# Optimization experiments

Hardware: AMD Instinct MI355X
Metric: run time of the kernel (lower is better)

The kernel has to match this reference:

```python
import jax, jax.numpy as jnp
import numpy as np

ALPHA = 0.1
BETA = 0.1
N_TASKS = 8
N_ROBOTS = 3
B = 2097152


def setup_inputs() -> dict:
    key = jax.random.key(0)
    k1, k2, k3, k4 = jax.random.split(key, 4)
    predictions = jax.random.normal(k1, (B, N_TASKS * N_ROBOTS), dtype=jnp.float32)
    targets = jax.random.uniform(k2, (B, N_TASKS * N_ROBOTS), dtype=jnp.float32)
    R = jax.random.uniform(k3, (B, N_TASKS, N_ROBOTS), dtype=jnp.float32)  # task capability requirements
    Q = jax.random.uniform(k4, (B, N_ROBOTS, N_ROBOTS), dtype=jnp.float32)  # per-robot capability rows
    return {"predictions": predictions, "targets": targets, "R": R, "Q": Q}


def reference(predictions, targets, R, Q):
    # BCEWithLogitsLoss (mean): softplus(x) - x * t
    base_loss = jnp.mean(jax.nn.softplus(predictions) - predictions * targets)

    b = predictions.shape[0]
    pred_m = predictions.reshape(b, N_TASKS, N_ROBOTS)  # [B, 8, 3]
    # robot assigned to task iff prediction > 0.5 (hard threshold, as in original)
    assigned = (pred_m > 0.5).astype(predictions.dtype)  # [B, 8, 3]
    # total capability per task: sum of Q rows of assigned robots
    total_capability = jnp.einsum('btr,brc->btc', assigned, Q)  # [B, 8, 3]
    shortage = jnp.maximum(R - total_capability, 0.0).sum(-1)  # [B, 8]
    # original only counts tasks where the raw prediction row-sum is > 0
    active = pred_m.sum(-1) > 0.0  # [B, 8]
    capability_violation = jnp.where(active, shortage, 0.0).sum() / b

    time_violation = jnp.asarray(0.0, dtype=predictions.dtype)
    total_loss = base_loss + ALPHA * capability_violation + BETA * time_violation
    return (total_loss, base_loss, capability_violation, time_violation)
```

## Files before the change

### kernel.cpp

```cpp
#include <hip/hip_runtime.h>

#define N_TASKS 8
#define ROW 24
#define ROWB 96
#define TILE 64
#define QROWB 36

typedef __attribute__((address_space(3))) void* lds_ptr_t;
typedef const __attribute__((address_space(1))) void* gbl_ptr_t;

#define PRED0 0
#define R0    512
#define Q0    1024
#define BUFSZ 1168

#define SB0 __builtin_amdgcn_sched_barrier(0)
#define WAITV25 do { asm volatile("s_waitcnt vmcnt(25)" ::: "memory"); } while (0)
#define WAITV0  do { asm volatile("s_waitcnt vmcnt(0)"  ::: "memory"); } while (0)

#define STAGE(TILEIDX, BSEL) do {                                              \
    const char* _predT = (const char*)pred + (size_t)(TILEIDX) * (TILE * ROWB);\
    const char* _RT    = (const char*)Rm   + (size_t)(TILEIDX) * (TILE * ROWB);\
    const char* _QT    = (const char*)Qm   + (size_t)(TILEIDX) * (TILE * QROWB);\
    _Pragma("unroll")                                                          \
    for (int _j = 0; _j < 8; ++_j)                                             \
        __builtin_amdgcn_global_load_lds((gbl_ptr_t)(_predT + _j * 768 + srcPR),\
                                         (lds_ptr_t)(&bufL[BSEL][PRED0 + _j * 64]), 16, 0, 0);\
    _Pragma("unroll")                                                          \
    for (int _j = 0; _j < 8; ++_j)                                             \
        __builtin_amdgcn_global_load_lds((gbl_ptr_t)(_RT + _j * 768 + srcPR),  \
                                         (lds_ptr_t)(&bufL[BSEL][R0 + _j * 64]), 16, 0, 0);\
    __builtin_amdgcn_global_load_lds((gbl_ptr_t)(_QT + l * 16),                \
                                     (lds_ptr_t)(&bufL[BSEL][Q0]), 16, 0, 0);  \
    __builtin_amdgcn_global_load_lds((gbl_ptr_t)(_QT + 1024 + l * 16),         \
                                     (lds_ptr_t)(&bufL[BSEL][Q0 + 64]), 16, 0, 0);\
    __builtin_amdgcn_global_load_lds((gbl_ptr_t)(_QT + 2048 + l * 4),          \
                                     (lds_ptr_t)(&bufL[BSEL][Q0 + 128]), 4, 0, 0);\
} while (0)

#define LOADT(TT, TILEIDX) do {                                                \
    const char* _targT = (const char*)targ + (size_t)(TILEIDX) * (TILE * ROWB);\
    _Pragma("unroll")                                                          \
    for (int _j = 0; _j < 6; ++_j)                                             \
        TT[_j] = *(const float4*)(_targT + (_j * 64 + l) * 16);                \
} while (0)

#define COMPUTE(BSEL, TT) do {                                                 \
    const float4* _predL = &bufL[BSEL][PRED0];                                 \
    const float4* _RL    = &bufL[BSEL][R0];                                    \
    const float* _qbase  = (const float*)&bufL[BSEL][Q0];                      \
    float pv[ROW];                                                             \
    _Pragma("unroll")                                                          \
    for (int _s = 0; _s < 6; ++_s) {                                           \
        float4 _v = _predL[8 * l + (_s ^ key)];                                \
        pv[4 * _s + 0] = _v.x; pv[4 * _s + 1] = _v.y;                          \
        pv[4 * _s + 2] = _v.z; pv[4 * _s + 3] = _v.w;                          \
    }                                                                          \
    float _sp0 = 0.0f, _sp1 = 0.0f;                                            \
    _Pragma("unroll")                                                          \
    for (int _i = 0; _i < ROW; _i += 2) {                                      \
        _sp0 += fmaxf(pv[_i],     0.0f) + __logf(1.0f + __expf(-fabsf(pv[_i])));\
        _sp1 += fmaxf(pv[_i + 1], 0.0f) + __logf(1.0f + __expf(-fabsf(pv[_i + 1])));\
    }                                                                          \
    float rv[ROW];                                                             \
    _Pragma("unroll")                                                          \
    for (int _s = 0; _s < 6; ++_s) {                                           \
        float4 _v = _RL[8 * l + (_s ^ key)];                                   \
        rv[4 * _s + 0] = _v.x; rv[4 * _s + 1] = _v.y;                          \
        rv[4 * _s + 2] = _v.z; rv[4 * _s + 3] = _v.w;                          \
    }                                                                          \
    float qv[9];                                                               \
    _Pragma("unroll")                                                          \
    for (int _e = 0; _e < 9; ++_e) qv[_e] = _qbase[9 * l + _e];                \
    float _cap = 0.0f;                                                         \
    _Pragma("unroll")                                                          \
    for (int _tk = 0; _tk < N_TASKS; ++_tk) {                                  \
        float _p0 = pv[_tk * 3 + 0];                                           \
        float _p1 = pv[_tk * 3 + 1];                                           \
        float _p2 = pv[_tk * 3 + 2];                                           \
        float _a0 = (_p0 > 0.5f) ? 1.0f : 0.0f;                                \
        float _a1 = (_p1 > 0.5f) ? 1.0f : 0.0f;                                \
        float _a2 = (_p2 > 0.5f) ? 1.0f : 0.0f;                                \
        float _tc0 = _a0 * qv[0] + _a1 * qv[3] + _a2 * qv[6];                  \
        float _tc1 = _a0 * qv[1] + _a1 * qv[4] + _a2 * qv[7];                  \
        float _tc2 = _a0 * qv[2] + _a1 * qv[5] + _a2 * qv[8];                  \
        float _sh  = fmaxf(rv[_tk * 3 + 0] - _tc0, 0.0f)                       \
                   + fmaxf(rv[_tk * 3 + 1] - _tc1, 0.0f)                       \
                   + fmaxf(rv[_tk * 3 + 2] - _tc2, 0.0f);                      \
        bool _active = (_p0 + _p1 + _p2) > 0.0f;                               \
        _cap += _active ? _sh : 0.0f;                                          \
    }                                                                          \
    float _dt0 = 0.0f, _dt1 = 0.0f;                                            \
    _Pragma("unroll")                                                          \
    for (int _j = 0; _j < 6; ++_j) {                                           \
        float4 _pw = _predL[pieceIdx[_j]];                                     \
        _dt0 += _pw.x * TT[_j].x + _pw.y * TT[_j].y;                           \
        _dt1 += _pw.z * TT[_j].z + _pw.w * TT[_j].w;                           \
    }                                                                          \
    base_acc += (double)((_sp0 + _sp1) - (_dt0 + _dt1));                       \
    cap_acc  += (double)_cap;                                                  \
} while (0)

__global__ __launch_bounds__(64) void mrta_partial_kernel(
    const float* __restrict__ pred,
    const float* __restrict__ targ,
    const float* __restrict__ Rm,
    const float* __restrict__ Qm,
    double* __restrict__ partials,
    int B)
{
    __shared__ __align__(16) float4 bufL[2][BUFSZ];

    const int l = threadIdx.x;

    int sfix = (l & 7) ^ (l >> 3);
    if (sfix >= 6) sfix = l & 1;
    const int srcPR = ROWB * (l >> 3) + 16 * sfix;

    int pieceIdx[6];
#pragma unroll
    for (int j = 0; j < 6; ++j) {
        int g = j * 64 + l;
        int r = g / 6;
        int s = g - r * 6;
        pieceIdx[j] = 8 * r + (s ^ (r & 7));
    }
    const int key = l & 7;

    double base_acc = 0.0, cap_acc = 0.0;

    const int G = gridDim.x;
    const int ntiles = B / TILE;
    const int t0 = blockIdx.x;
    const int n = (t0 < ntiles) ? ((ntiles - t0 + G - 1) / G) : 0;

    float4 ttA[6], ttB[6];

    if (n > 0) { STAGE(t0, 0); LOADT(ttA, t0); }

    for (int i = 0; i < n; i += 2) {
        const int tcur = t0 + i * G;
        {
            if (i + 1 < n) {
                const int tnext = tcur + G;
                STAGE(tnext, 1); LOADT(ttB, tnext);
                SB0; WAITV25; SB0;
            } else {
                SB0; WAITV0; SB0;
            }
            COMPUTE(0, ttA);
            SB0;
        }
        if (i + 1 < n) {
            if (i + 2 < n) {
                const int tnn = tcur + 2 * G;
                STAGE(tnn, 0); LOADT(ttA, tnn);
                SB0; WAITV25; SB0;
            } else {
                SB0; WAITV0; SB0;
            }
            COMPUTE(1, ttB);
            SB0;
        }
    }

    if (blockIdx.x == 0) {
        int row = ntiles * TILE + l;
        if (row < B) {
            const float* pr = pred + (size_t)row * ROW;
            const float* tr = targ + (size_t)row * ROW;
            const float* rr = Rm   + (size_t)row * ROW;
            const float* qr = Qm   + (size_t)row * 9;
            float base = 0.0f;
            float pv[ROW];
            for (int i = 0; i < ROW; ++i) {
                float x = pr[i];
                pv[i] = x;
                base += fmaxf(x, 0.0f) + __logf(1.0f + __expf(-fabsf(x))) - x * tr[i];
            }
            float cap = 0.0f;
            for (int tk = 0; tk < N_TASKS; ++tk) {
                float p0 = pv[tk * 3 + 0], p1 = pv[tk * 3 + 1], p2 = pv[tk * 3 + 2];
                float a0 = (p0 > 0.5f) ? 1.0f : 0.0f;
                float a1 = (p1 > 0.5f) ? 1.0f : 0.0f;
                float a2 = (p2 > 0.5f) ? 1.0f : 0.0f;
                float tc0 = a0 * qr[0] + a1 * qr[3] + a2 * qr[6];
                float tc1 = a0 * qr[1] + a1 * qr[4] + a2 * qr[7];
                float tc2 = a0 * qr[2] + a1 * qr[5] + a2 * qr[8];
                float sh  = fmaxf(rr[tk * 3 + 0] - tc0, 0.0f)
                          + fmaxf(rr[tk * 3 + 1] - tc1, 0.0f)
                          + fmaxf(rr[tk * 3 + 2] - tc2, 0.0f);
                if ((p0 + p1 + p2) > 0.0f) cap += sh;
            }
            base_acc += (double)base;
            cap_acc  += (double)cap;
        }
    }

#pragma unroll
    for (int off = 32; off > 0; off >>= 1) {
        base_acc += __shfl_down(base_acc, off);
        cap_acc  += __shfl_down(cap_acc, off);
    }
    if (l == 0) {
        partials[blockIdx.x]             = base_acc;
        partials[gridDim.x + blockIdx.x] = cap_acc;
    }
}

__global__ __launch_bounds__(256) void mrta_final_kernel(
    const double* __restrict__ partials,
    int nparts,
    float* __restrict__ out,
    double inv_BM,
    double inv_B)
{
    double b = 0.0, c = 0.0;
    for (int i = threadIdx.x; i < nparts; i += 256) {
        b += partials[i];
        c += partials[nparts + i];
    }
#pragma unroll
    for (int off = 32; off > 0; off >>= 1) {
        b += __shfl_down(b, off);
        c += __shfl_down(c, off);
    }
    __shared__ double sb[4];
    __shared__ double sc[4];
    const int wave = threadIdx.x >> 6;
    const int lane = threadIdx.x & 63;
    if (lane == 0) { sb[wave] = b; sc[wave] = c; }
    __syncthreads();
    if (threadIdx.x == 0) {
        double bsum = sb[0] + sb[1] + sb[2] + sb[3];
        double csum = sc[0] + sc[1] + sc[2] + sc[3];
        double base = bsum * inv_BM;
        double cap  = csum * inv_B;
        double tot  = base + 0.1 * cap;
        out[0] = (float)tot;
        out[1] = (float)base;
        out[2] = (float)cap;
        out[3] = 0.0f;
    }
}

extern "C" void kernel_launch(void* const* d_in, const int* in_sizes, int n_in,
                              void* d_out, int out_size, void* d_ws, size_t ws_size,
                              hipStream_t stream) {
    const float* pred = (const float*)d_in[0];
    const float* targ = (const float*)d_in[1];
    const float* Rm   = (const float*)d_in[2];
    const float* Qm   = (const float*)d_in[3];
    float* out = (float*)d_out;

    const int B = in_sizes[0] / ROW;

    int blocks = 2048;
    if ((size_t)(2 * blocks) * sizeof(double) > ws_size) {
        blocks = (int)(ws_size / (2 * sizeof(double)));
        if (blocks > 2048) blocks = 2048;
        if (blocks < 1) blocks = 1;
    }

    double* partials = (double*)d_ws;

    mrta_partial_kernel<<<blocks, 64, 0, stream>>>(pred, targ, Rm, Qm, partials, B);
    mrta_final_kernel<<<1, 256, 0, stream>>>(partials, blocks, out,
                                             1.0 / ((double)B * ROW),
                                             1.0 / (double)B);
}
```

Measured before the change: 124.9 us.

## Replace async global-to-LDS staging with register prefetch and contiguous tile ranges

Drops the double-buffered global_load_lds staging with manual vmcnt waits. Each tile's pred, targets, R and Q are now loaded into registers, one tile ahead. Only pred, R and Q are then written to a single swizzled LDS buffer for the per-row capability pass, while the BCE term is computed straight from the coalesced register copies. Blocks now own contiguous tile ranges instead of a grid stride, the grid is doubled to 4096, and launch bounds request 2 waves per SIMD. This raises register pressure and drops the explicit overlap control, in exchange for simpler scheduling and possibly better DRAM locality and occupancy.

```diff
diff --git a/kernel.cpp b/kernel.cpp
--- a/kernel.cpp
+++ b/kernel.cpp
@@ -6,72 +6,66 @@
 #define TILE 64
 #define QROWB 36
 
-typedef __attribute__((address_space(3))) void* lds_ptr_t;
-typedef const __attribute__((address_space(1))) void* gbl_ptr_t;
-
 #define PRED0 0
 #define R0    512
 #define Q0    1024
-#define BUFSZ 1168
-
-#define SB0 __builtin_amdgcn_sched_barrier(0)
-#define WAITV25 do { asm volatile("s_waitcnt vmcnt(25)" ::: "memory"); } while (0)
-#define WAITV0  do { asm volatile("s_waitcnt vmcnt(0)"  ::: "memory"); } while (0)
-
-#define STAGE(TILEIDX, BSEL) do {                                              \
-    const char* _predT = (const char*)pred + (size_t)(TILEIDX) * (TILE * ROWB);\
-    const char* _RT    = (const char*)Rm   + (size_t)(TILEIDX) * (TILE * ROWB);\
-    const char* _QT    = (const char*)Qm   + (size_t)(TILEIDX) * (TILE * QROWB);\
-    _Pragma("unroll")                                                          \
-    for (int _j = 0; _j < 8; ++_j)                                             \
-        __builtin_amdgcn_global_load_lds((gbl_ptr_t)(_predT + _j * 768 + srcPR),\
-                                         (lds_ptr_t)(&bufL[BSEL][PRED0 + _j * 64]), 16, 0, 0);\
-    _Pragma("unroll")                                                          \
-    for (int _j = 0; _j < 8; ++_j)                                             \
-        __builtin_amdgcn_global_load_lds((gbl_ptr_t)(_RT + _j * 768 + srcPR),  \
-                                         (lds_ptr_t)(&bufL[BSEL][R0 + _j * 64]), 16, 0, 0);\
-    __builtin_amdgcn_global_load_lds((gbl_ptr_t)(_QT + l * 16),                \
-                                     (lds_ptr_t)(&bufL[BSEL][Q0]), 16, 0, 0);  \
-    __builtin_amdgcn_global_load_lds((gbl_ptr_t)(_QT + 1024 + l * 16),         \
-                                     (lds_ptr_t)(&bufL[BSEL][Q0 + 64]), 16, 0, 0);\
-    __builtin_amdgcn_global_load_lds((gbl_ptr_t)(_QT + 2048 + l * 4),          \
-                                     (lds_ptr_t)(&bufL[BSEL][Q0 + 128]), 4, 0, 0);\
-} while (0)
-
-#define LOADT(TT, TILEIDX) do {                                                \
-    const char* _targT = (const char*)targ + (size_t)(TILEIDX) * (TILE * ROWB);\
-    _Pragma("unroll")                                                          \
-    for (int _j = 0; _j < 6; ++_j)                                             \
-        TT[_j] = *(const float4*)(_targT + (_j * 64 + l) * 16);                \
-} while (0)
-
-#define COMPUTE(BSEL, TT) do {                                                 \
-    const float4* _predL = &bufL[BSEL][PRED0];                                 \
-    const float4* _RL    = &bufL[BSEL][R0];                                    \
-    const float* _qbase  = (const float*)&bufL[BSEL][Q0];                      \
-    float pv[ROW];                                                             \
+#define LDSN  1168
+
+#define LOADSET(P, T, RR, Q, TI) do {                                          \
+    const char* _p = (const char*)pred + (size_t)(TI) * (TILE * ROWB);         \
+    const char* _t = (const char*)targ + (size_t)(TI) * (TILE * ROWB);         \
+    const char* _r = (const char*)Rm   + (size_t)(TI) * (TILE * ROWB);         \
+    const char* _q = (const char*)Qm   + (size_t)(TI) * (TILE * QROWB);        \
+    _Pragma("unroll")                                                          \
+    for (int _j = 0; _j < 6; ++_j) {                                           \
+        P[_j]  = *(const float4*)(_p + (_j * 64 + l) * 16);                    \
+        T[_j]  = *(const float4*)(_t + (_j * 64 + l) * 16);                    \
+        RR[_j] = *(const float4*)(_r + (_j * 64 + l) * 16);                    \
+    }                                                                          \
+    Q[0] = *(const float4*)(_q + l * 16);                                      \
+    Q[1] = *(const float4*)(_q + (64 + l) * 16);                               \
+    Q[2] = *(const float4*)(_q + (128 + (l & 15)) * 16);                       \
+} while (0)
+
+#define STORESET(P, RR, Q) do {                                                \
+    _Pragma("unroll")                                                          \
+    for (int _j = 0; _j < 6; ++_j) {                                           \
+        lds[PRED0 + waddr[_j]] = P[_j];                                        \
+        lds[R0    + waddr[_j]] = RR[_j];                                       \
+    }                                                                          \
+    lds[Q0 + l]      = Q[0];                                                   \
+    lds[Q0 + 64 + l] = Q[1];                                                   \
+    if (l < 16) lds[Q0 + 128 + l] = Q[2];                                      \
+} while (0)
+
+#define FLATSET(P, T) do {                                                     \
+    float _f0 = 0.0f, _f1 = 0.0f;                                              \
+    _Pragma("unroll")                                                          \
+    for (int _j = 0; _j < 6; ++_j) {                                           \
+        float4 _x = P[_j], _y = T[_j];                                         \
+        _f0 += fmaxf(_x.x, 0.0f) + __logf(1.0f + __expf(-fabsf(_x.x))) - _x.x * _y.x; \
+        _f1 += fmaxf(_x.y, 0.0f) + __logf(1.0f + __expf(-fabsf(_x.y))) - _x.y * _y.y; \
+        _f0 += fmaxf(_x.z, 0.0f) + __logf(1.0f + __expf(-fabsf(_x.z))) - _x.z * _y.z; \
+        _f1 += fmaxf(_x.w, 0.0f) + __logf(1.0f + __expf(-fabsf(_x.w))) - _x.w * _y.w; \
+    }                                                                          \
+    base_acc += (double)(_f0 + _f1);                                           \
+} while (0)
+
+#define ROWCAP() do {                                                          \
+    float pv[ROW], rv[ROW];                                                    \
     _Pragma("unroll")                                                          \
     for (int _s = 0; _s < 6; ++_s) {                                           \
-        float4 _v = _predL[8 * l + (_s ^ key)];                                \
+        float4 _v = lds[PRED0 + 8 * l + (_s ^ key)];                           \
         pv[4 * _s + 0] = _v.x; pv[4 * _s + 1] = _v.y;                          \
         pv[4 * _s + 2] = _v.z; pv[4 * _s + 3] = _v.w;                          \
-    }                                                                          \
-    float _sp0 = 0.0f, _sp1 = 0.0f;                                            \
-    _Pragma("unroll")                                                          \
-    for (int _i = 0; _i < ROW; _i += 2) {                                      \
-        _sp0 += fmaxf(pv[_i],     0.0f) + __logf(1.0f + __expf(-fabsf(pv[_i])));\
-        _sp1 += fmaxf(pv[_i + 1], 0.0f) + __logf(1.0f + __expf(-fabsf(pv[_i + 1])));\
-    }                                                                          \
-    float rv[ROW];                                                             \
-    _Pragma("unroll")                                                          \
-    for (int _s = 0; _s < 6; ++_s) {                                           \
-        float4 _v = _RL[8 * l + (_s ^ key)];                                   \
-        rv[4 * _s + 0] = _v.x; rv[4 * _s + 1] = _v.y;                          \
-        rv[4 * _s + 2] = _v.z; rv[4 * _s + 3] = _v.w;                          \
-    }                                                                          \
+        float4 _w = lds[R0 + 8 * l + (_s ^ key)];                              \
+        rv[4 * _s + 0] = _w.x; rv[4 * _s + 1] = _w.y;                          \
+        rv[4 * _s + 2] = _w.z; rv[4 * _s + 3] = _w.w;                          \
+    }                                                                          \
+    const float* _qf = (const float*)&lds[Q0];                                 \
     float qv[9];                                                               \
     _Pragma("unroll")                                                          \
-    for (int _e = 0; _e < 9; ++_e) qv[_e] = _qbase[9 * l + _e];                \
+    for (int _e = 0; _e < 9; ++_e) qv[_e] = _qf[9 * l + _e];                   \
     float _cap = 0.0f;                                                         \
     _Pragma("unroll")                                                          \
     for (int _tk = 0; _tk < N_TASKS; ++_tk) {                                  \
@@ -90,18 +84,10 @@
         bool _active = (_p0 + _p1 + _p2) > 0.0f;                               \
         _cap += _active ? _sh : 0.0f;                                          \
     }                                                                          \
-    float _dt0 = 0.0f, _dt1 = 0.0f;                                            \
-    _Pragma("unroll")                                                          \
-    for (int _j = 0; _j < 6; ++_j) {                                           \
-        float4 _pw = _predL[pieceIdx[_j]];                                     \
-        _dt0 += _pw.x * TT[_j].x + _pw.y * TT[_j].y;                           \
-        _dt1 += _pw.z * TT[_j].z + _pw.w * TT[_j].w;                           \
-    }                                                                          \
-    base_acc += (double)((_sp0 + _sp1) - (_dt0 + _dt1));                       \
-    cap_acc  += (double)_cap;                                                  \
-} while (0)
-
-__global__ __launch_bounds__(64) void mrta_partial_kernel(
+    cap_acc += (double)_cap;                                                   \
+} while (0)
+
+__global__ __launch_bounds__(64, 2) void mrta_partial_kernel(
     const float* __restrict__ pred,
     const float* __restrict__ targ,
     const float* __restrict__ Rm,
@@ -109,59 +95,47 @@
     double* __restrict__ partials,
     int B)
 {
-    __shared__ __align__(16) float4 bufL[2][BUFSZ];
+    __shared__ __align__(16) float4 lds[LDSN];
 
     const int l = threadIdx.x;
 
-    int sfix = (l & 7) ^ (l >> 3);
-    if (sfix >= 6) sfix = l & 1;
-    const int srcPR = ROWB * (l >> 3) + 16 * sfix;
-
-    int pieceIdx[6];
+    int waddr[6];
 #pragma unroll
     for (int j = 0; j < 6; ++j) {
-        int g = j * 64 + l;
-        int r = g / 6;
-        int s = g - r * 6;
-        pieceIdx[j] = 8 * r + (s ^ (r & 7));
+        int g = 64 * j + l;
+        int r = g / 6, s = g - 6 * r;
+        waddr[j] = 8 * r + (s ^ (r & 7));
     }
     const int key = l & 7;
 
     double base_acc = 0.0, cap_acc = 0.0;
 
+    const int ntiles = B / TILE;
     const int G = gridDim.x;
-    const int ntiles = B / TILE;
-    const int t0 = blockIdx.x;
-    const int n = (t0 < ntiles) ? ((ntiles - t0 + G - 1) / G) : 0;
-
-    float4 ttA[6], ttB[6];
-
-    if (n > 0) { STAGE(t0, 0); LOADT(ttA, t0); }
-
-    for (int i = 0; i < n; i += 2) {
-        const int tcur = t0 + i * G;
-        {
-            if (i + 1 < n) {
-                const int tnext = tcur + G;
-                STAGE(tnext, 1); LOADT(ttB, tnext);
-                SB0; WAITV25; SB0;
-            } else {
-                SB0; WAITV0; SB0;
-            }
-            COMPUTE(0, ttA);
-            SB0;
-        }
-        if (i + 1 < n) {
-            if (i + 2 < n) {
-                const int tnn = tcur + 2 * G;
-                STAGE(tnn, 0); LOADT(ttA, tnn);
-                SB0; WAITV25; SB0;
-            } else {
-                SB0; WAITV0; SB0;
-            }
-            COMPUTE(1, ttB);
-            SB0;
-        }
+    const int tpb = ntiles / G, rem = ntiles % G;
+    const int start = blockIdx.x * tpb + (blockIdx.x < rem ? blockIdx.x : rem);
+    const int cnt = tpb + (blockIdx.x < rem ? 1 : 0);
+
+    float4 pA[6], tA[6], rA[6], qA[3];
+    float4 pB[6], tB[6], rB[6], qB[3];
+
+    if (cnt > 0) LOADSET(pA, tA, rA, qA, start);
+
+    int i = 0;
+    for (; i + 2 <= cnt; i += 2) {
+        STORESET(pA, rA, qA);
+        LOADSET(pB, tB, rB, qB, start + i + 1);
+        FLATSET(pA, tA);
+        ROWCAP();
+        STORESET(pB, rB, qB);
+        if (i + 2 < cnt) LOADSET(pA, tA, rA, qA, start + i + 2);
+        FLATSET(pB, tB);
+        ROWCAP();
+    }
+    if (i < cnt) {
+        STORESET(pA, rA, qA);
+        FLATSET(pA, tA);
+        ROWCAP();
     }
 
     if (blockIdx.x == 0) {
@@ -173,10 +147,10 @@
             const float* qr = Qm   + (size_t)row * 9;
             float base = 0.0f;
             float pv[ROW];
-            for (int i = 0; i < ROW; ++i) {
-                float x = pr[i];
-                pv[i] = x;
-                base += fmaxf(x, 0.0f) + __logf(1.0f + __expf(-fabsf(x))) - x * tr[i];
+            for (int k = 0; k < ROW; ++k) {
+                float x = pr[k];
+                pv[k] = x;
+                base += fmaxf(x, 0.0f) + __logf(1.0f + __expf(-fabsf(x))) - x * tr[k];
             }
             float cap = 0.0f;
             for (int tk = 0; tk < N_TASKS; ++tk) {
@@ -255,10 +229,10 @@
 
     const int B = in_sizes[0] / ROW;
 
-    int blocks = 2048;
+    int blocks = 4096;
     if ((size_t)(2 * blocks) * sizeof(double) > ws_size) {
         blocks = (int)(ws_size / (2 * sizeof(double)));
-        if (blocks > 2048) blocks = 2048;
+        if (blocks > 4096) blocks = 4096;
         if (blocks < 1) blocks = 1;
     }
 
```

Result: slower. 181.9 us (+45.7%).
